# Kernel tuning notes

Measured on AMD Instinct MI355X. Metric: run time of the kernel, lower is better.

The kernel has to match this reference:

```python
import jax, jax.numpy as jnp
import numpy as np

BN_EPS = 1e-5
NORM_EPS = 1e-6


def _nearest_resize(m, H, W):
    # torch F.interpolate(mode='nearest'): idx = floor(i * in/out)
    B, C, h, w = m.shape
    iy = (jnp.arange(H) * h) // H
    ix = (jnp.arange(W) * w) // W
    return m[:, :, iy][:, :, :, ix]


def _distance_transform(m_s):
    # Euclidean distance of every pixel to nearest foreground pixel (mask>0.5),
    # normalized per-sample to [0,1]; all-background samples -> ones map.
    B, _, H, W = m_s.shape
    HW = H * W
    yy, xx = jnp.meshgrid(jnp.arange(H, dtype=jnp.float32),
                          jnp.arange(W, dtype=jnp.float32), indexing='ij')
    ys, xs = yy.reshape(-1), xx.reshape(-1)
    # shared [HW, HW] pairwise squared distances (same for all batch elems)
    D2 = (ys[:, None] - ys[None, :]) ** 2 + (xs[:, None] - xs[None, :]) ** 2
    fg = m_s.reshape(B, HW) > 0.5                                  # [B, HW]
    min_d2 = jnp.min(jnp.where(fg[:, None, :], D2[None], jnp.inf), axis=-1)  # [B, HW]
    has_fg = fg.any(axis=1, keepdims=True)
    dist = jnp.where(has_fg, jnp.sqrt(min_d2), 1.0)
    mx = dist.max(axis=1, keepdims=True)
    dist = dist / (mx + NORM_EPS)
    return dist.reshape(B, 1, H, W)


def _forward(f_s, supp_feat_bin, support_mask, w_fusion, gamma, beta):
    B, C, H, W = f_s.shape
    m_s = _nearest_resize(support_mask, H, W)
    attn = jax.nn.sigmoid(jnp.sum(f_s * supp_feat_bin, axis=1, keepdims=True))  # [B,1,H,W]
    f_w = f_s * attn
    dist = _distance_transform(m_s)
    fusion_in = jnp.concatenate([f_s, supp_feat_bin, f_w, dist], axis=1)  # [B,3C+1,H,W]
    y = jnp.einsum('oc,bchw->bohw', w_fusion, fusion_in)  # 1x1 conv, no bias
    # BatchNorm2d in training mode: biased batch stats over (B,H,W)
    mean = y.mean(axis=(0, 2, 3))
    var = y.var(axis=(0, 2, 3))
    yn = (y - mean[None, :, None, None]) * jax.lax.rsqrt(var[None, :, None, None] + BN_EPS)
    return jax.nn.relu(yn * gamma[None, :, None, None] + beta[None, :, None, None])


def setup_inputs() -> dict:
    key = jax.random.key(0)
    k1, k2, k3, k4 = jax.random.split(key, 4)
    B, C, H, W = 8, 256, 64, 64
    Hm, Wm = 256, 256
    return {
        'f_s': jax.random.normal(k1, (B, C, H, W), dtype=jnp.float32),
        'supp_feat_bin': jax.random.normal(k2, (B, C, H, W), dtype=jnp.float32),
        'support_mask': jax.random.uniform(k3, (B, 1, Hm, Wm), dtype=jnp.float32),
        'w_fusion': jax.random.normal(k4, (C, 3 * C + 1), dtype=jnp.float32) * 0.02,
        'gamma': jnp.ones((C,), dtype=jnp.float32),
        'beta': jnp.zeros((C,), dtype=jnp.float32),
    }


def reference(f_s, supp_feat_bin, support_mask, w_fusion, gamma, beta):
    return _forward(f_s, supp_feat_bin, support_mask, w_fusion, gamma, beta)
```

## Files before the change

### kernel.cpp

```cpp
#include <hip/hip_runtime.h>
#include <math.h>

#define C_IN   256
#define HW_    4096
#define KW_    769
#define NPIX_BN 32768.0f

typedef short bf16x8 __attribute__((ext_vector_type(8)));
typedef float f32x4  __attribute__((ext_vector_type(4)));
typedef unsigned short u16x8 __attribute__((ext_vector_type(8)));

__device__ inline unsigned short f2bf(float x){
    unsigned u = __float_as_uint(x);
    u += 0x7fffu + ((u >> 16) & 1u);
    return (unsigned short)(u >> 16);
}
__device__ inline float bf2f(unsigned short h){
    return __uint_as_float(((unsigned)h) << 16);
}

__global__ __launch_bounds__(256) void prep_w(
    const float* __restrict__ w, unsigned short* __restrict__ wp)
{
    int idx = blockIdx.x * 256 + threadIdx.x;
    int j  = idx & 7;
    int o  = (idx >> 3) & 255;
    int t2 = idx >> 11;
    int c  = (t2 >> 2) * 32 + (t2 & 3) * 8 + j;
    wp[idx] = f2bf(w[(size_t)o * KW_ + c]);
}

__global__ __launch_bounds__(256) void conv_kernel(
    const float* __restrict__ f_s, const float* __restrict__ sfb,
    unsigned short* __restrict__ xf, unsigned short* __restrict__ xs,
    unsigned short* __restrict__ xw)
{
    __shared__ float red[4][64];
    __shared__ float attn_sm[64];
    int blk = blockIdx.x;
    int t = threadIdx.x, lane = t & 63, g = t >> 6;
    int b = blk >> 6;
    int p = (blk & 63) * 64 + lane;
    const float* fB = f_s + (size_t)b * C_IN * HW_ + p;
    const float* sB = sfb + (size_t)b * C_IN * HW_ + p;
    u16x8* XF = (u16x8*)xf;
    u16x8* XS = (u16x8*)xs;
    u16x8* XW = (u16x8*)xw;

    float ap = 0.f;
    u16x8 xfreg[8];
    float fv[8], sv[8], fv2[8], sv2[8];
    #pragma unroll
    for (int j = 0; j < 8; ++j) {
        fv[j] = fB[(size_t)(g * 8 + j) * HW_];
        sv[j] = sB[(size_t)(g * 8 + j) * HW_];
    }
    #pragma unroll
    for (int ks = 0; ks < 8; ++ks) {
        if (ks < 7) {
            #pragma unroll
            for (int j = 0; j < 8; ++j) {
                fv2[j] = fB[(size_t)((ks + 1) * 32 + g * 8 + j) * HW_];
                sv2[j] = sB[(size_t)((ks + 1) * 32 + g * 8 + j) * HW_];
            }
        }
        u16x8 pf, ps;
        #pragma unroll
        for (int j = 0; j < 8; ++j) {
            ap += fv[j] * sv[j];
            pf[j] = f2bf(fv[j]);
            ps[j] = f2bf(sv[j]);
        }
        int plane = (b * 8 + ks) * 4 + g;
        XF[(size_t)plane * HW_ + p] = pf;
        XS[(size_t)plane * HW_ + p] = ps;
        xfreg[ks] = pf;
        #pragma unroll
        for (int j = 0; j < 8; ++j) { fv[j] = fv2[j]; sv[j] = sv2[j]; }
    }
    red[g][lane] = ap;
    __syncthreads();
    if (t < 64) {
        float a = red[0][t] + red[1][t] + red[2][t] + red[3][t];
        attn_sm[t] = 1.f / (1.f + __expf(-a));
    }
    __syncthreads();
    float at = attn_sm[lane];
    #pragma unroll
    for (int ks = 0; ks < 8; ++ks) {
        u16x8 pw;
        #pragma unroll
        for (int j = 0; j < 8; ++j)
            pw[j] = f2bf(bf2f(xfreg[ks][j]) * at);
        XW[(size_t)((b * 8 + ks) * 4 + g) * HW_ + p] = pw;
    }
}

__global__ __launch_bounds__(512) void dist_kernel(
    const float* __restrict__ mask, float* __restrict__ dist_raw,
    unsigned* __restrict__ dmax)
{
    __shared__ unsigned fg[4096];
    __shared__ int cnt;
    __shared__ float wmax[8];
    int b = blockIdx.x, tile = blockIdx.y;
    int t = threadIdx.x, lane = t & 63;
    if (t == 0) cnt = 0;
    __syncthreads();
    const float* mb = mask + (size_t)b * 65536;
    #pragma unroll
    for (int r = 0; r < 8; ++r) {
        int pp = r * 512 + t;
        int i = pp >> 6, j = pp & 63;
        bool pred = mb[i * 1024 + j * 4] > 0.5f;
        unsigned long long bal = __ballot(pred);
        int base = 0;
        if (lane == 0) base = atomicAdd(&cnt, __popcll(bal));
        base = __shfl(base, 0, 64);
        if (pred)
            fg[base + __popcll(bal & ((1ull << lane) - 1ull))] =
                (unsigned)((i << 8) | j);
    }
    __syncthreads();
    int nfg = cnt;
    int pix = tile * 128 + (t >> 2);
    int q = t & 3;
    int py = pix >> 6, px = pix & 63;
    int md = 0x7fffffff;
    #pragma unroll 4
    for (int it = q; it < nfg; it += 4) {
        unsigned e = fg[it];
        int dy = py - (int)(e >> 8);
        int dx = px - (int)(e & 255u);
        int d2 = dy * dy + dx * dx;
        md = min(md, d2);
    }
    md = min(md, __shfl_xor(md, 1, 64));
    md = min(md, __shfl_xor(md, 2, 64));
    float d = (nfg == 0) ? 1.0f : sqrtf((float)md);
    if (q == 0) dist_raw[b * HW_ + pix] = d;
    float mm = d;
    #pragma unroll
    for (int off = 1; off < 64; off <<= 1)
        mm = fmaxf(mm, __shfl_xor(mm, off, 64));
    if (lane == 0) wmax[t >> 6] = mm;
    __syncthreads();
    if (t == 0) {
        float M = wmax[0];
        #pragma unroll
        for (int i = 1; i < 8; ++i) M = fmaxf(M, wmax[i]);
        atomicMax(dmax + b, __float_as_uint(M));
    }
}

__global__ __launch_bounds__(256) void gemm_kernel(
    const unsigned short* __restrict__ xf, const unsigned short* __restrict__ xs,
    const unsigned short* __restrict__ xw, const unsigned short* __restrict__ wprep,
    const float* __restrict__ w,
    const float* __restrict__ dist_raw, const unsigned* __restrict__ dmax,
    unsigned short* __restrict__ ybf,
    float* __restrict__ gsum, float* __restrict__ gsumsq)
{
    int bx = blockIdx.x;
    int ot = bx & 1, nt = bx >> 1;
    int oBase = ot * 128, nBase = nt * 128;
    int b = nBase >> 12, pBase = nBase & 4095;
    int t = threadIdx.x, lane = t & 63, g = t >> 6;
    int wo = g >> 1, wn = g & 1;
    int l15 = lane & 15, kq = lane >> 4;
    int oW = oBase + wo * 64;
    int pix0 = pBase + wn * 64 + l15;

    const bf16x8* WP  = (const bf16x8*)wprep;
    const bf16x8* XFp = (const bf16x8*)xf;
    const bf16x8* XSp = (const bf16x8*)xs;
    const bf16x8* XWp = (const bf16x8*)xw;

    f32x4 acc[4][4];
    #pragma unroll
    for (int fo = 0; fo < 4; ++fo)
        #pragma unroll
        for (int fn = 0; fn < 4; ++fn)
            acc[fo][fn] = (f32x4){0.f, 0.f, 0.f, 0.f};

    bf16x8 aC[4], xC[4];
    #pragma unroll
    for (int fn = 0; fn < 4; ++fn)
        xC[fn] = XFp[(size_t)((b * 8 + 0) * 4 + kq) * HW_ + pix0 + fn * 16];
    #pragma unroll
    for (int fo = 0; fo < 4; ++fo)
        aC[fo] = WP[(0 * 4 + kq) * 256 + oW + fo * 16 + l15];

    #pragma unroll
    for (int ks = 0; ks < 24; ++ks) {
        bf16x8 aN[4], xN[4];
        if (ks < 23) {
            int kn = ks + 1, mn = kn >> 3, k8 = kn & 7;
            const bf16x8* Xp = (mn == 0) ? XFp : ((mn == 1) ? XSp : XWp);
            #pragma unroll
            for (int fn = 0; fn < 4; ++fn)
                xN[fn] = Xp[(size_t)((b * 8 + k8) * 4 + kq) * HW_ + pix0 + fn * 16];
            #pragma unroll
            for (int fo = 0; fo < 4; ++fo)
                aN[fo] = WP[(kn * 4 + kq) * 256 + oW + fo * 16 + l15];
        }
        #pragma unroll
        for (int fo = 0; fo < 4; ++fo)
            #pragma unroll
            for (int fn = 0; fn < 4; ++fn)
                acc[fo][fn] = __builtin_amdgcn_mfma_f32_16x16x32_bf16(
                    aC[fo], xC[fn], acc[fo][fn], 0, 0, 0);
        if (ks < 23) {
            #pragma unroll
            for (int i = 0; i < 4; ++i) { aC[i] = aN[i]; xC[i] = xN[i]; }
        }
    }

    float dinv = 1.0f / (__uint_as_float(dmax[b]) + 1e-6f);
    const float* dR = dist_raw + b * HW_ + pBase + wn * 64;
    float dn[4];
    #pragma unroll
    for (int fn = 0; fn < 4; ++fn)
        dn[fn] = dR[fn * 16 + l15] * dinv;

    float s_acc[4][4], ss_acc[4][4];
    #pragma unroll
    for (int fo = 0; fo < 4; ++fo) {
        #pragma unroll
        for (int r = 0; r < 4; ++r) {
            int o = oW + fo * 16 + kq * 4 + r;
            float wd = w[(size_t)o * KW_ + 768];
            float s = 0.f, ss = 0.f;
            #pragma unroll
            for (int fn = 0; fn < 4; ++fn) {
                float v = acc[fo][fn][r] + wd * dn[fn];
                ybf[((size_t)(b * C_IN + o)) * HW_ + pBase + wn * 64 + fn * 16 + l15] = f2bf(v);
                s += v; ss += v * v;
            }
            s_acc[fo][r] = s; ss_acc[fo][r] = ss;
        }
    }
    #pragma unroll
    for (int m = 8; m; m >>= 1) {
        #pragma unroll
        for (int fo = 0; fo < 4; ++fo)
            #pragma unroll
            for (int r = 0; r < 4; ++r) {
                s_acc[fo][r]  += __shfl_xor(s_acc[fo][r],  m, 64);
                ss_acc[fo][r] += __shfl_xor(ss_acc[fo][r], m, 64);
            }
    }
    if (l15 == 0) {
        #pragma unroll
        for (int fo = 0; fo < 4; ++fo)
            #pragma unroll
            for (int r = 0; r < 4; ++r) {
                int o = oW + fo * 16 + kq * 4 + r;
                atomicAdd(&gsum[o],   s_acc[fo][r]);
                atomicAdd(&gsumsq[o], ss_acc[fo][r]);
            }
    }
}

__global__ __launch_bounds__(256) void bn_kernel(
    const float* __restrict__ gsum, const float* __restrict__ gsumsq,
    const float* __restrict__ gamma, const float* __restrict__ beta,
    const unsigned short* __restrict__ ybf, float* __restrict__ out)
{
    int bo = blockIdx.x;
    int o = bo & 255;
    float mean = gsum[o] * (1.0f / NPIX_BN);
    float var  = gsumsq[o] * (1.0f / NPIX_BN) - mean * mean;
    float sc = gamma[o] * rsqrtf(var + 1e-5f);
    float sh = beta[o] - mean * sc;
    const u16x8* yp = (const u16x8*)(ybf + (size_t)bo * HW_);
    float4* op = (float4*)(out + (size_t)bo * HW_);
    int t = threadIdx.x;
    #pragma unroll
    for (int r = 0; r < 2; ++r) {
        u16x8 v = yp[r * 256 + t];
        float4 lo, hi;
        lo.x = fmaxf(bf2f(v[0]) * sc + sh, 0.f);
        lo.y = fmaxf(bf2f(v[1]) * sc + sh, 0.f);
        lo.z = fmaxf(bf2f(v[2]) * sc + sh, 0.f);
        lo.w = fmaxf(bf2f(v[3]) * sc + sh, 0.f);
        hi.x = fmaxf(bf2f(v[4]) * sc + sh, 0.f);
        hi.y = fmaxf(bf2f(v[5]) * sc + sh, 0.f);
        hi.z = fmaxf(bf2f(v[6]) * sc + sh, 0.f);
        hi.w = fmaxf(bf2f(v[7]) * sc + sh, 0.f);
        op[(r * 256 + t) * 2]     = lo;
        op[(r * 256 + t) * 2 + 1] = hi;
    }
}

extern "C" void kernel_launch(void* const* d_in, const int* in_sizes, int n_in,
                              void* d_out, int out_size, void* d_ws, size_t ws_size,
                              hipStream_t stream)
{
    const float* f_s   = (const float*)d_in[0];
    const float* sfb   = (const float*)d_in[1];
    const float* mask  = (const float*)d_in[2];
    const float* w     = (const float*)d_in[3];
    const float* gamma = (const float*)d_in[4];
    const float* beta  = (const float*)d_in[5];
    float* out = (float*)d_out;
    float* ws  = (float*)d_ws;

    float*          dist_raw = ws;
    unsigned*       dmax     = (unsigned*)(ws + 32768);
    float*          gsum     = ws + 32784;
    float*          gsumsq   = ws + 33040;
    unsigned short* wprep    = (unsigned short*)(ws + 33296);

    const size_t P1_need = ((size_t)131600 + 4 * 4194304) * 4;
    unsigned short *xf, *xs, *xw, *ybf;
    if (ws_size >= P1_need) {
        xf  = (unsigned short*)(ws + 131600);
        xs  = (unsigned short*)(ws + 131600 + 1 * (size_t)4194304);
        xw  = (unsigned short*)(ws + 131600 + 2 * (size_t)4194304);
        ybf = (unsigned short*)(ws + 131600 + 3 * (size_t)4194304);
    } else {
        xf  = (unsigned short*)d_out;
        xs  = ((unsigned short*)d_out) + 8388608;
        xw  = (unsigned short*)(ws + 131600);
        ybf = (unsigned short*)(ws + 131600 + (size_t)4194304);
    }

    hipMemsetAsync(ws + 32768, 0, (33296 - 32768) * 4, stream);

    prep_w<<<768, 256, 0, stream>>>(w, wprep);
    conv_kernel<<<512, 256, 0, stream>>>(f_s, sfb, xf, xs, xw);
    dist_kernel<<<dim3(8, 32), 512, 0, stream>>>(mask, dist_raw, dmax);
    gemm_kernel<<<512, 256, 0, stream>>>(xf, xs, xw, wprep, w, dist_raw,
                                         dmax, ybf, gsum, gsumsq);
    bn_kernel<<<2048, 256, 0, stream>>>(gsum, gsumsq, gamma, beta, ybf, out);
}
```

Measured before the change: 234.1 us.

## Halve GEMM pixel tile, double grid, and deepen register prefetch pipeline

The GEMM block tile shrinks from 128x128 to 128x64 (output channels by pixels), so the kernel launches 1024 blocks instead of 512. Register prefetch becomes deeper, with two A buffers and three X buffers rotated across a 6-step unrolled schedule. A launch-bounds occupancy hint of 4 is added. The aim is better latency hiding and fuller use of the GPU for this memory-streaming GEMM, at the cost of more weight reloads per output and more atomics for the BN statistics.

```diff
diff --git a/kernel.cpp b/kernel.cpp
--- a/kernel.cpp
+++ b/kernel.cpp
@@ -153,7 +153,7 @@
     }
 }
 
-__global__ __launch_bounds__(256) void gemm_kernel(
+__global__ __launch_bounds__(256, 4) void gemm_kernel(
     const unsigned short* __restrict__ xf, const unsigned short* __restrict__ xs,
     const unsigned short* __restrict__ xw, const unsigned short* __restrict__ wprep,
     const float* __restrict__ w,
@@ -163,64 +163,70 @@
 {
     int bx = blockIdx.x;
     int ot = bx & 1, nt = bx >> 1;
-    int oBase = ot * 128, nBase = nt * 128;
+    int oBase = ot * 128, nBase = nt * 64;
     int b = nBase >> 12, pBase = nBase & 4095;
     int t = threadIdx.x, lane = t & 63, g = t >> 6;
     int wo = g >> 1, wn = g & 1;
     int l15 = lane & 15, kq = lane >> 4;
     int oW = oBase + wo * 64;
-    int pix0 = pBase + wn * 64 + l15;
+    int pix0 = pBase + wn * 32 + l15;
 
     const bf16x8* WP  = (const bf16x8*)wprep;
     const bf16x8* XFp = (const bf16x8*)xf;
     const bf16x8* XSp = (const bf16x8*)xs;
     const bf16x8* XWp = (const bf16x8*)xw;
 
-    f32x4 acc[4][4];
+    f32x4 acc[4][2];
     #pragma unroll
     for (int fo = 0; fo < 4; ++fo)
         #pragma unroll
-        for (int fn = 0; fn < 4; ++fn)
+        for (int fn = 0; fn < 2; ++fn)
             acc[fo][fn] = (f32x4){0.f, 0.f, 0.f, 0.f};
 
-    bf16x8 aC[4], xC[4];
-    #pragma unroll
-    for (int fn = 0; fn < 4; ++fn)
-        xC[fn] = XFp[(size_t)((b * 8 + 0) * 4 + kq) * HW_ + pix0 + fn * 16];
-    #pragma unroll
-    for (int fo = 0; fo < 4; ++fo)
-        aC[fo] = WP[(0 * 4 + kq) * 256 + oW + fo * 16 + l15];
-
-    #pragma unroll
-    for (int ks = 0; ks < 24; ++ks) {
-        bf16x8 aN[4], xN[4];
-        if (ks < 23) {
-            int kn = ks + 1, mn = kn >> 3, k8 = kn & 7;
-            const bf16x8* Xp = (mn == 0) ? XFp : ((mn == 1) ? XSp : XWp);
-            #pragma unroll
-            for (int fn = 0; fn < 4; ++fn)
-                xN[fn] = Xp[(size_t)((b * 8 + k8) * 4 + kq) * HW_ + pix0 + fn * 16];
-            #pragma unroll
-            for (int fo = 0; fo < 4; ++fo)
-                aN[fo] = WP[(kn * 4 + kq) * 256 + oW + fo * 16 + l15];
-        }
-        #pragma unroll
-        for (int fo = 0; fo < 4; ++fo)
-            #pragma unroll
-            for (int fn = 0; fn < 4; ++fn)
-                acc[fo][fn] = __builtin_amdgcn_mfma_f32_16x16x32_bf16(
-                    aC[fo], xC[fn], acc[fo][fn], 0, 0, 0);
-        if (ks < 23) {
-            #pragma unroll
-            for (int i = 0; i < 4; ++i) { aC[i] = aN[i]; xC[i] = xN[i]; }
-        }
-    }
+    bf16x8 aP0[4], aP1[4], xP0[2], xP1[2], xP2[2];
+
+#define LOADA(kn, dst) { \
+    const bf16x8* _wp = WP + ((kn) * 4 + kq) * 256 + oW + l15; \
+    dst[0] = _wp[0]; dst[1] = _wp[16]; dst[2] = _wp[32]; dst[3] = _wp[48]; }
+
+#define LOADX(kn, dst) { \
+    const bf16x8* _xp = ((kn) < 8 ? XFp : ((kn) < 16 ? XSp : XWp)) \
+        + (size_t)((b * 8 + ((kn) & 7)) * 4 + kq) * HW_ + pix0; \
+    dst[0] = _xp[0]; dst[1] = _xp[16]; }
+
+#define MFMA8(A, X) { \
+    _Pragma("unroll") \
+    for (int fo = 0; fo < 4; ++fo) { \
+        acc[fo][0] = __builtin_amdgcn_mfma_f32_16x16x32_bf16(A[fo], X[0], acc[fo][0], 0, 0, 0); \
+        acc[fo][1] = __builtin_amdgcn_mfma_f32_16x16x32_bf16(A[fo], X[1], acc[fo][1], 0, 0, 0); } }
+
+#define STEP(kn, A, X) { \
+    MFMA8(A, X); \
+    if ((kn) + 2 < 24) LOADA((kn) + 2, A); \
+    if ((kn) + 3 < 24) LOADX((kn) + 3, X); }
+
+    LOADX(0, xP0); LOADX(1, xP1); LOADX(2, xP2);
+    LOADA(0, aP0); LOADA(1, aP1);
+
+    #pragma unroll
+    for (int kb = 0; kb < 24; kb += 6) {
+        STEP(kb + 0, aP0, xP0);
+        STEP(kb + 1, aP1, xP1);
+        STEP(kb + 2, aP0, xP2);
+        STEP(kb + 3, aP1, xP0);
+        STEP(kb + 4, aP0, xP1);
+        STEP(kb + 5, aP1, xP2);
+    }
+#undef STEP
+#undef MFMA8
+#undef LOADX
+#undef LOADA
 
     float dinv = 1.0f / (__uint_as_float(dmax[b]) + 1e-6f);
-    const float* dR = dist_raw + b * HW_ + pBase + wn * 64;
-    float dn[4];
-    #pragma unroll
-    for (int fn = 0; fn < 4; ++fn)
+    const float* dR = dist_raw + b * HW_ + pBase + wn * 32;
+    float dn[2];
+    #pragma unroll
+    for (int fn = 0; fn < 2; ++fn)
         dn[fn] = dR[fn * 16 + l15] * dinv;
 
     float s_acc[4][4], ss_acc[4][4];
@@ -232,9 +238,9 @@
             float wd = w[(size_t)o * KW_ + 768];
             float s = 0.f, ss = 0.f;
             #pragma unroll
-            for (int fn = 0; fn < 4; ++fn) {
+            for (int fn = 0; fn < 2; ++fn) {
                 float v = acc[fo][fn][r] + wd * dn[fn];
-                ybf[((size_t)(b * C_IN + o)) * HW_ + pBase + wn * 64 + fn * 16 + l15] = f2bf(v);
+                ybf[((size_t)(b * C_IN + o)) * HW_ + pBase + wn * 32 + fn * 16 + l15] = f2bf(v);
                 s += v; ss += v * v;
             }
             s_acc[fo][r] = s; ss_acc[fo][r] = ss;
@@ -331,7 +337,7 @@
     prep_w<<<768, 256, 0, stream>>>(w, wprep);
     conv_kernel<<<512, 256, 0, stream>>>(f_s, sfb, xf, xs, xw);
     dist_kernel<<<dim3(8, 32), 512, 0, stream>>>(mask, dist_raw, dmax);
-    gemm_kernel<<<512, 256, 0, stream>>>(xf, xs, xw, wprep, w, dist_raw,
-                                         dmax, ybf, gsum, gsumsq);
+    gemm_kernel<<<1024, 256, 0, stream>>>(xf, xs, xw, wprep, w, dist_raw,
+                                          dmax, ybf, gsum, gsumsq);
     bn_kernel<<<2048, 256, 0, stream>>>(gsum, gsumsq, gamma, beta, ybf, out);
 }
```

Measured after the change: 277.0 us. +18.3%, slower.

## Stage GEMM operand tiles in LDS via direct global-to-LDS loads

Applied to the files above, without the earlier changes.

Replaces the per-wave register double-buffered global loads in the bf16 MFMA GEMM with cooperative global_load_lds transfers into shared memory. Each k-step loads the block's 128x32 weight and pixel tiles once, and all four waves then read their fragments from LDS. This removes the duplicate global reads that different waves made for the same tiles. In exchange it drops the register prefetch pipeline and adds two barriers per k-step, so load latency is no longer overlapped with MFMA work.

```diff
diff --git a/kernel.cpp b/kernel.cpp
--- a/kernel.cpp
+++ b/kernel.cpp
@@ -18,6 +18,11 @@
 __device__ inline float bf2f(unsigned short h){
     return __uint_as_float(((unsigned)h) << 16);
 }
+
+#define GLOAD16(gp, lp) \
+    __builtin_amdgcn_global_load_lds( \
+        (const __attribute__((address_space(1))) void*)(gp), \
+        (__attribute__((address_space(3))) void*)(lp), 16, 0, 0)
 
 __global__ __launch_bounds__(256) void prep_w(
     const float* __restrict__ w, unsigned short* __restrict__ wp)
@@ -161,6 +166,9 @@
     unsigned short* __restrict__ ybf,
     float* __restrict__ gsum, float* __restrict__ gsumsq)
 {
+    __shared__ u16x8 LA[512];
+    __shared__ u16x8 LX[512];
+
     int bx = blockIdx.x;
     int ot = bx & 1, nt = bx >> 1;
     int oBase = ot * 128, nBase = nt * 128;
@@ -169,12 +177,21 @@
     int wo = g >> 1, wn = g & 1;
     int l15 = lane & 15, kq = lane >> 4;
     int oW = oBase + wo * 64;
-    int pix0 = pBase + wn * 64 + l15;
-
-    const bf16x8* WP  = (const bf16x8*)wprep;
-    const bf16x8* XFp = (const bf16x8*)xf;
-    const bf16x8* XSp = (const bf16x8*)xs;
-    const bf16x8* XWp = (const bf16x8*)xw;
+
+    const u16x8* WPc = (const u16x8*)wprep;
+    const u16x8* XFc = (const u16x8*)xf;
+    const u16x8* XSc = (const u16x8*)xs;
+    const u16x8* XWc = (const u16x8*)xw;
+    const bf16x8* LAr = (const bf16x8*)LA;
+    const bf16x8* LXr = (const bf16x8*)LX;
+
+    int kq0 = t >> 7;
+    int kq1 = 2 + (t >> 7);
+    int rl  = t & 127;
+    u16x8* dstA0 = &LA[g * 64];
+    u16x8* dstA1 = &LA[256 + g * 64];
+    u16x8* dstX0 = &LX[g * 64];
+    u16x8* dstX1 = &LX[256 + g * 64];
 
     f32x4 acc[4][4];
     #pragma unroll
@@ -183,37 +200,29 @@
         for (int fn = 0; fn < 4; ++fn)
             acc[fo][fn] = (f32x4){0.f, 0.f, 0.f, 0.f};
 
-    bf16x8 aC[4], xC[4];
-    #pragma unroll
-    for (int fn = 0; fn < 4; ++fn)
-        xC[fn] = XFp[(size_t)((b * 8 + 0) * 4 + kq) * HW_ + pix0 + fn * 16];
-    #pragma unroll
-    for (int fo = 0; fo < 4; ++fo)
-        aC[fo] = WP[(0 * 4 + kq) * 256 + oW + fo * 16 + l15];
-
-    #pragma unroll
-    for (int ks = 0; ks < 24; ++ks) {
-        bf16x8 aN[4], xN[4];
-        if (ks < 23) {
-            int kn = ks + 1, mn = kn >> 3, k8 = kn & 7;
-            const bf16x8* Xp = (mn == 0) ? XFp : ((mn == 1) ? XSp : XWp);
-            #pragma unroll
-            for (int fn = 0; fn < 4; ++fn)
-                xN[fn] = Xp[(size_t)((b * 8 + k8) * 4 + kq) * HW_ + pix0 + fn * 16];
-            #pragma unroll
-            for (int fo = 0; fo < 4; ++fo)
-                aN[fo] = WP[(kn * 4 + kq) * 256 + oW + fo * 16 + l15];
-        }
+    #pragma unroll
+    for (int kn = 0; kn < 24; ++kn) {
+        int k8 = kn & 7;
+        const u16x8* Xsel = (kn < 8) ? XFc : ((kn < 16) ? XSc : XWc);
+        GLOAD16(WPc + (kn * 4 + kq0) * 256 + oBase + rl, dstA0);
+        GLOAD16(WPc + (kn * 4 + kq1) * 256 + oBase + rl, dstA1);
+        GLOAD16(Xsel + (size_t)((b * 8 + k8) * 4 + kq0) * HW_ + pBase + rl, dstX0);
+        GLOAD16(Xsel + (size_t)((b * 8 + k8) * 4 + kq1) * HW_ + pBase + rl, dstX1);
+        __syncthreads();
+        bf16x8 af[4], xr[4];
+        #pragma unroll
+        for (int fo = 0; fo < 4; ++fo)
+            af[fo] = LAr[kq * 128 + wo * 64 + fo * 16 + l15];
+        #pragma unroll
+        for (int fn = 0; fn < 4; ++fn)
+            xr[fn] = LXr[kq * 128 + wn * 64 + fn * 16 + l15];
         #pragma unroll
         for (int fo = 0; fo < 4; ++fo)
             #pragma unroll
             for (int fn = 0; fn < 4; ++fn)
                 acc[fo][fn] = __builtin_amdgcn_mfma_f32_16x16x32_bf16(
-                    aC[fo], xC[fn], acc[fo][fn], 0, 0, 0);
-        if (ks < 23) {
-            #pragma unroll
-            for (int i = 0; i < 4; ++i) { aC[i] = aN[i]; xC[i] = xN[i]; }
-        }
+                    af[fo], xr[fn], acc[fo][fn], 0, 0, 0);
+        __syncthreads();
     }
 
     float dinv = 1.0f / (__uint_as_float(dmax[b]) + 1e-6f);
```

New measurement: 229.2 us. 1.02x faster.
